# Performance work log

Hardware: AMD Instinct MI355X
Metric: run time of the kernel (lower is better)

Reference implementation:

```python
import jax, jax.numpy as jnp
import numpy as np

DIM = 1024
NUM_HEADS = 16
HEAD_DIM = DIM // NUM_HEADS
SCALE = HEAD_DIM ** -0.5


def setup_inputs() -> dict:
    key = jax.random.key(0)
    k1, k2, k3, k4 = jax.random.split(key, 4)
    x = jax.random.normal(k1, (4, 2048, DIM), dtype=jnp.float32)
    # torch nn.Linear(dim, 3*dim, bias=False): weight shape [3*dim, dim]
    w_qkv = jax.random.normal(k2, (3 * DIM, DIM), dtype=jnp.float32) * (DIM ** -0.5)
    # torch nn.Linear(dim, dim): weight [dim, dim], bias [dim]
    w_proj = jax.random.normal(k3, (DIM, DIM), dtype=jnp.float32) * (DIM ** -0.5)
    b_proj = jax.random.normal(k4, (DIM,), dtype=jnp.float32) * 0.01
    return {"x": x, "w_qkv": w_qkv, "w_proj": w_proj, "b_proj": b_proj}


def reference(x, w_qkv, w_proj, b_proj):
    B, N, C = x.shape
    # qkv: [B, N, 3*C] -> [3, B, H, N, Dh]
    qkv = (x @ w_qkv.T).reshape(B, N, 3, NUM_HEADS, HEAD_DIM)
    qkv = jnp.transpose(qkv, (2, 0, 3, 1, 4))
    q, k, v = qkv[0], qkv[1], qkv[2]
    # full score matrix, as in the original module
    attn = jnp.einsum("bhqd,bhkd->bhqk", q, k) * SCALE
    attn = jax.nn.softmax(attn, axis=-1)
    out = jnp.einsum("bhqk,bhkd->bhqd", attn, v)  # [B,H,N,Dh]
    out = jnp.transpose(out, (0, 2, 1, 3)).reshape(B, N, C)
    return out @ w_proj.T + b_proj
```

## Files before the change

kernel.cpp:

```cpp
#include <hip/hip_runtime.h>
#include <stdint.h>

#define DIM 1024
#define SEQ 2048
#define BATCH 4
#define ROWS (BATCH*SEQ)
#define QSCALE 0.1803368801111f

typedef __attribute__((ext_vector_type(8))) short bf16x8;
typedef __attribute__((ext_vector_type(4))) float f32x4;
typedef __attribute__((ext_vector_type(8))) _Float16 f16x8;
typedef __attribute__((ext_vector_type(2))) __fp16 fp16x2_raw;

#if __has_builtin(__builtin_amdgcn_exp2f)
#define EXP2F(x) __builtin_amdgcn_exp2f(x)
#else
#define EXP2F(x) __expf((x) * 0.69314718056f)
#endif

#define MFMA_BF16_K32(a,b,c) __builtin_amdgcn_mfma_f32_16x16x32_bf16(a,b,c,0,0,0)
#define MFMA_F16_K32(a,b,c)  __builtin_amdgcn_mfma_f32_16x16x32_f16(a,b,c,0,0,0)

__device__ __forceinline__ unsigned short f2bf(float f) {
  union { float f; unsigned int u; } v; v.f = f;
  unsigned int u = v.u;
  return (unsigned short)((u + 0x7FFFu + ((u >> 16) & 1u)) >> 16);
}

__device__ __forceinline__ unsigned short f2h(float f) {
  union { _Float16 h; unsigned short u; } v;
  v.h = (_Float16)f;
  return v.u;
}

__device__ __forceinline__ unsigned int pkrtz_bits(float lo, float hi) {
  union { fp16x2_raw h; unsigned int u; } v;
  v.h = __builtin_amdgcn_cvt_pkrtz(lo, hi);
  return v.u;
}

__device__ __forceinline__ void gload_lds16(const void* g, void* l) {
  __builtin_amdgcn_global_load_lds(
      (const __attribute__((address_space(1))) unsigned int*)g,
      (__attribute__((address_space(3))) unsigned int*)l,
      16, 0, 0);
}

__global__ void cast_all(const float* __restrict__ x,
                         const float* __restrict__ wq,
                         const float* __restrict__ wp,
                         unsigned short* __restrict__ xb,
                         unsigned short* __restrict__ wqb,
                         unsigned short* __restrict__ wpb) {
  const int i = (blockIdx.x * blockDim.x + threadIdx.x) * 4;
  const float* src;
  unsigned short* dst;
  int off;
  if (i < ROWS * DIM)                 { src = x;  dst = xb;  off = i; }
  else if (i < ROWS * DIM + 3 * DIM * DIM) { src = wq; dst = wqb; off = i - ROWS * DIM; }
  else                                { src = wp; dst = wpb; off = i - ROWS * DIM - 3 * DIM * DIM; }
  float4 f = *(const float4*)(src + off);
  ushort4 o;
  o.x = f2bf(f.x); o.y = f2bf(f.y); o.z = f2bf(f.z); o.w = f2bf(f.w);
  *(ushort4*)(dst + off) = o;
}

__global__ __launch_bounds__(256) void gemm_qkv(
    const unsigned short* __restrict__ A,
    const unsigned short* __restrict__ W,
    unsigned short* __restrict__ qb,
    unsigned short* __restrict__ kb,
    unsigned short* __restrict__ vtb) {
  const int K = DIM;
  __shared__ unsigned short Al[128 * 32];
  __shared__ unsigned short Wl[128 * 32];
  const int tid  = threadIdx.x;
  const int wave = tid >> 6, lane = tid & 63;
  const int quad = lane >> 4, l16 = lane & 15;
  const int m0 = blockIdx.y * 128, n0 = blockIdx.x * 128;
  const int wr = (wave >> 1) * 64, wc = (wave & 1) * 64;
  const int which = n0 >> 10;

  f32x4 acc[4][4];
#pragma unroll
  for (int i = 0; i < 4; i++)
#pragma unroll
    for (int j = 0; j < 4; j++) acc[i][j] = (f32x4)0.f;

  const int arow = wave * 16 + (lane >> 2);
  const int acol = (lane & 3) * 8;
  const unsigned short* Ag = A + (size_t)(m0 + arow) * K + acol;
  const unsigned short* Wg = W + (size_t)(n0 + arow) * K + acol;

  if (which < 2) {
    for (int kt = 0; kt < K; kt += 32) {
      __syncthreads();
#pragma unroll
      for (int i = 0; i < 2; i++) {
        gload_lds16((const void*)(Ag + (size_t)(i * 64) * K + kt), (void*)&Al[i * 2048 + wave * 512]);
        gload_lds16((const void*)(Wg + (size_t)(i * 64) * K + kt), (void*)&Wl[i * 2048 + wave * 512]);
      }
      __syncthreads();
      bf16x8 af[4], wf[4];
#pragma unroll
      for (int i = 0; i < 4; i++) {
        af[i] = *(const bf16x8*)&Al[(wr + i * 16 + l16) * 32 + quad * 8];
        wf[i] = *(const bf16x8*)&Wl[(wc + i * 16 + l16) * 32 + quad * 8];
      }
#pragma unroll
      for (int i = 0; i < 4; i++)
#pragma unroll
        for (int j = 0; j < 4; j++)
          acc[i][j] = __builtin_amdgcn_mfma_f32_16x16x32_bf16(wf[j], af[i], acc[i][j], 0, 0, 0);
    }
    const float sc = (which == 0) ? QSCALE : 1.f;
    unsigned short* base = (which == 0) ? qb : kb;
#pragma unroll
    for (int i = 0; i < 4; i++) {
      const int tok = m0 + wr + i * 16 + l16;
      const int b = tok >> 11, n = tok & 2047;
#pragma unroll
      for (int j = 0; j < 4; j++) {
        const int col0 = n0 + wc + j * 16 + quad * 4;
        const int h = (col0 >> 6) & 15, d = col0 & 63;
        ushort4 o4;
        o4.x = f2bf(acc[i][j][0] * sc); o4.y = f2bf(acc[i][j][1] * sc);
        o4.z = f2bf(acc[i][j][2] * sc); o4.w = f2bf(acc[i][j][3] * sc);
        *(ushort4*)&base[((size_t)(b * 16 + h) * SEQ + n) * 64 + d] = o4;
      }
    }
  } else {
    for (int kt = 0; kt < K; kt += 32) {
      __syncthreads();
#pragma unroll
      for (int i = 0; i < 2; i++) {
        gload_lds16((const void*)(Ag + (size_t)(i * 64) * K + kt), (void*)&Al[i * 2048 + wave * 512]);
        gload_lds16((const void*)(Wg + (size_t)(i * 64) * K + kt), (void*)&Wl[i * 2048 + wave * 512]);
      }
      __syncthreads();
      bf16x8 af[4], wf[4];
#pragma unroll
      for (int i = 0; i < 4; i++) {
        af[i] = *(const bf16x8*)&Al[(wr + i * 16 + l16) * 32 + quad * 8];
        wf[i] = *(const bf16x8*)&Wl[(wc + i * 16 + l16) * 32 + quad * 8];
      }
#pragma unroll
      for (int i = 0; i < 4; i++)
#pragma unroll
        for (int j = 0; j < 4; j++)
          acc[i][j] = __builtin_amdgcn_mfma_f32_16x16x32_bf16(af[i], wf[j], acc[i][j], 0, 0, 0);
    }
#pragma unroll
    for (int i = 0; i < 4; i++) {
      const int row = m0 + wr + i * 16 + quad * 4;
      const int b = row >> 11, n = row & 2047;
#pragma unroll
      for (int j = 0; j < 4; j++) {
        const int col = n0 + wc + j * 16 + l16;
        const int h = (col >> 6) & 15, d = col & 63;
        ushort4 o4;
        o4.x = f2h(acc[i][j][0]); o4.y = f2h(acc[i][j][1]);
        o4.z = f2h(acc[i][j][2]); o4.w = f2h(acc[i][j][3]);
        *(ushort4*)&vtb[((size_t)(b * 16 + h) * 64 + d) * SEQ + n] = o4;
      }
    }
  }
}

__global__ __launch_bounds__(256, 2) void attn_kernel(
    const unsigned short* __restrict__ qb,
    const unsigned short* __restrict__ kb,
    const unsigned short* __restrict__ vtb,
    unsigned short* __restrict__ out) {
  __shared__ unsigned short Kl[2][64 * 64];
  __shared__ unsigned short Vl[2][64 * 64];

  const int tid  = threadIdx.x;
  const int wave = tid >> 6, lane = tid & 63;
  const int quad = lane >> 4, l16 = lane & 15;
  const int bh    = blockIdx.x;
  const int qtile = blockIdx.y;
  const size_t qkbase = (size_t)bh * SEQ * 64;
  const int q0 = qtile * 256 + wave * 64;

  bf16x8 qf[4][2];
#pragma unroll
  for (int mi = 0; mi < 4; mi++)
#pragma unroll
    for (int kk = 0; kk < 2; kk++)
      qf[mi][kk] = *(const bf16x8*)&qb[qkbase + (size_t)(q0 + mi * 16 + l16) * 64 + kk * 32 + quad * 8];

  f32x4 o[4][4];
#pragma unroll
  for (int mi = 0; mi < 4; mi++)
#pragma unroll
    for (int nt = 0; nt < 4; nt++) o[mi][nt] = (f32x4)0.f;
  f32x4 lacc[4];
#pragma unroll
  for (int mi = 0; mi < 4; mi++) lacc[mi] = (f32x4)0.f;

  union { f16x8 v; unsigned int d[4]; } ones8;
#pragma unroll
  for (int j = 0; j < 4; j++) ones8.d[j] = 0x3C003C00u;

  const unsigned short* Kg = kb + qkbase;
  const unsigned short* Vg = vtb + (size_t)bh * 64 * SEQ;
  const int srow = tid >> 3;
  const int schk = tid & 7;
  const int swK = (srow & 3) | (((srow >> 3) & 1) << 2);
  const int swV = srow & 7;

  auto stage = [&](int kt, int buf) {
#pragma unroll
    for (int p = 0; p < 2; p++) {
      const int r = p * 32 + srow;
      gload_lds16((const void*)(Kg + (size_t)(kt + r) * 64 + (schk ^ swK) * 8),
                  (void*)&Kl[buf][p * 2048 + wave * 512]);
      gload_lds16((const void*)(Vg + (size_t)r * SEQ + kt + (schk ^ swV) * 8),
                  (void*)&Vl[buf][p * 2048 + wave * 512]);
    }
  };

  stage(0, 0);

  const int rbase = ((l16 >> 2) << 3) + (l16 & 3);
  const int sR = (l16 & 3) | (((l16 >> 2) & 1) << 2);

  int buf = 0;
  for (int kt = 0; kt < SEQ; kt += 64, buf ^= 1) {
    __syncthreads();
    if (kt + 64 < SEQ) stage(kt + 64, buf ^ 1);

#pragma unroll
    for (int kk = 0; kk < 2; kk++) {
      bf16x8 kf[2][2];
#pragma unroll
      for (int T = 0; T < 2; T++) {
        const int R = kk * 32 + rbase + 4 * T;
        kf[T][0] = *(const bf16x8*)&Kl[buf][R * 64 + ((quad ^ sR) << 3)];
        kf[T][1] = *(const bf16x8*)&Kl[buf][R * 64 + (((4 + quad) ^ sR) << 3)];
      }
      f16x8 vf[4];
#pragma unroll
      for (int nt = 0; nt < 4; nt++) {
        const int vr = nt * 16 + l16;
        vf[nt] = *(const f16x8*)&Vl[buf][vr * 64 + (((kk * 4 + quad) ^ (vr & 7)) << 3)];
      }
#pragma unroll
      for (int mi = 0; mi < 4; mi++) {
        f32x4 s0 = (f32x4)0.f, s1 = (f32x4)0.f;
        s0 = MFMA_BF16_K32(kf[0][0], qf[mi][0], s0);
        s0 = MFMA_BF16_K32(kf[0][1], qf[mi][1], s0);
        s1 = MFMA_BF16_K32(kf[1][0], qf[mi][0], s1);
        s1 = MFMA_BF16_K32(kf[1][1], qf[mi][1], s1);
        union { f16x8 v; unsigned int d[4]; } pu;
        pu.d[0] = pkrtz_bits(EXP2F(s0[0]), EXP2F(s0[1]));
        pu.d[1] = pkrtz_bits(EXP2F(s0[2]), EXP2F(s0[3]));
        pu.d[2] = pkrtz_bits(EXP2F(s1[0]), EXP2F(s1[1]));
        pu.d[3] = pkrtz_bits(EXP2F(s1[2]), EXP2F(s1[3]));
        lacc[mi] = MFMA_F16_K32(pu.v, ones8.v, lacc[mi]);
#pragma unroll
        for (int nt = 0; nt < 4; nt++)
          o[mi][nt] = MFMA_F16_K32(pu.v, vf[nt], o[mi][nt]);
      }
    }
  }

  const int h = bh & 15, b = bh >> 4;
#pragma unroll
  for (int mi = 0; mi < 4; mi++) {
    float inv[4];
#pragma unroll
    for (int r = 0; r < 4; r++) inv[r] = 1.f / lacc[mi][r];
#pragma unroll
    for (int nt = 0; nt < 4; nt++)
#pragma unroll
      for (int r = 0; r < 4; r++)
        out[((size_t)(b * SEQ + q0 + mi * 16 + quad * 4 + r)) * DIM + h * 64 + nt * 16 + l16] =
            f2bf(o[mi][nt][r] * inv[r]);
  }
}

__global__ __launch_bounds__(256) void gemm_proj(
    const unsigned short* __restrict__ A,
    const unsigned short* __restrict__ W,
    float* __restrict__ out,
    const float* __restrict__ bias) {
  const int N = DIM, K = DIM;
  __shared__ unsigned short Al[128 * 32];
  __shared__ unsigned short Wl[128 * 32];
  const int tid  = threadIdx.x;
  const int wave = tid >> 6, lane = tid & 63;
  const int quad = lane >> 4, l16 = lane & 15;
  const int m0 = blockIdx.y * 128, n0 = blockIdx.x * 128;
  const int wr = (wave >> 1) * 64, wc = (wave & 1) * 64;

  f32x4 acc[4][4];
#pragma unroll
  for (int i = 0; i < 4; i++)
#pragma unroll
    for (int j = 0; j < 4; j++) acc[i][j] = (f32x4)0.f;

  const int arow = wave * 16 + (lane >> 2);
  const int acol = (lane & 3) * 8;
  const unsigned short* Ag = A + (size_t)(m0 + arow) * K + acol;
  const unsigned short* Wg = W + (size_t)(n0 + arow) * K + acol;

  for (int kt = 0; kt < K; kt += 32) {
    __syncthreads();
#pragma unroll
    for (int i = 0; i < 2; i++) {
      gload_lds16((const void*)(Ag + (size_t)(i * 64) * K + kt), (void*)&Al[i * 2048 + wave * 512]);
      gload_lds16((const void*)(Wg + (size_t)(i * 64) * K + kt), (void*)&Wl[i * 2048 + wave * 512]);
    }
    __syncthreads();

    bf16x8 af[4], wf[4];
#pragma unroll
    for (int i = 0; i < 4; i++) {
      af[i] = *(const bf16x8*)&Al[(wr + i * 16 + l16) * 32 + quad * 8];
      wf[i] = *(const bf16x8*)&Wl[(wc + i * 16 + l16) * 32 + quad * 8];
    }
#pragma unroll
    for (int i = 0; i < 4; i++)
#pragma unroll
      for (int j = 0; j < 4; j++)
        acc[i][j] = __builtin_amdgcn_mfma_f32_16x16x32_bf16(af[i], wf[j], acc[i][j], 0, 0, 0);
  }

#pragma unroll
  for (int i = 0; i < 4; i++) {
    const int row = m0 + wr + i * 16 + quad * 4;
#pragma unroll
    for (int j = 0; j < 4; j++) {
      const int col = n0 + wc + j * 16 + l16;
      const float bv = bias[col];
#pragma unroll
      for (int r = 0; r < 4; r++)
        out[(size_t)(row + r) * N + col] = acc[i][j][r] + bv;
    }
  }
}

extern "C" void kernel_launch(void* const* d_in, const int* in_sizes, int n_in,
                              void* d_out, int out_size, void* d_ws, size_t ws_size,
                              hipStream_t stream) {
  const float* x      = (const float*)d_in[0];
  const float* w_qkv  = (const float*)d_in[1];
  const float* w_proj = (const float*)d_in[2];
  const float* b_proj = (const float*)d_in[3];
  float* outp = (float*)d_out;

  char* ws = (char*)d_ws;
  unsigned short* xb     = (unsigned short*)(ws);
  unsigned short* wqkvb  = (unsigned short*)(ws + (16u << 20));
  unsigned short* wprojb = (unsigned short*)(ws + (22u << 20));
  unsigned short* qb     = (unsigned short*)(ws + (24u << 20));
  unsigned short* kb     = (unsigned short*)(ws + (40u << 20));
  unsigned short* vtb    = (unsigned short*)(ws + (56u << 20));
  unsigned short* aout   = (unsigned short*)(ws + (72u << 20));

  const int total4 = (ROWS * DIM + 3 * DIM * DIM + DIM * DIM) / 4;
  cast_all<<<total4 / 256, 256, 0, stream>>>(x, w_qkv, w_proj, xb, wqkvb, wprojb);

  gemm_qkv<<<dim3(24, 64), 256, 0, stream>>>(xb, wqkvb, qb, kb, vtb);
  attn_kernel<<<dim3(64, 8), 256, 0, stream>>>(qb, kb, vtb, aout);
  gemm_proj<<<dim3(8, 64), 256, 0, stream>>>(aout, wprojb, outp, b_proj);
}
```

Measured before the change: 257.5 us.

## Rewrite QKV GEMM with 256x256 tiles, double-buffered LDS, swizzle and ping-pong

Replaces the 128x128 single-buffer QKV GEMM with a 512-thread kernel using 256x256 tiles, K-step 64, double-buffered XOR-swizzled LDS, interleaved staging of the next tiles between MFMA phases, s_setprio, and a grouped block-index remap. Q/K and V parts are split into two template launches so that the branch is resolved at compile time. This aims to raise MFMA utilisation and hide global load latency in the largest GEMM. In exchange it uses large LDS (128KB per block) and many accumulator registers, and it adds a second kernel launch.

```diff
diff --git a/kernel.cpp b/kernel.cpp
--- a/kernel.cpp
+++ b/kernel.cpp
@@ -65,102 +65,197 @@
   *(ushort4*)(dst + off) = o;
 }
 
-__global__ __launch_bounds__(256) void gemm_qkv(
+template<int SWAP>
+__device__ __forceinline__ f32x4 mm(bf16x8 a, bf16x8 b, f32x4 c) {
+  if constexpr (SWAP) return __builtin_amdgcn_mfma_f32_16x16x32_bf16(b, a, c, 0, 0, 0);
+  else                return __builtin_amdgcn_mfma_f32_16x16x32_bf16(a, b, c, 0, 0, 0);
+}
+
+template<int SWAP, int NTX>
+__global__ __launch_bounds__(512, 2) void gemm_qkv8(
     const unsigned short* __restrict__ A,
     const unsigned short* __restrict__ W,
     unsigned short* __restrict__ qb,
     unsigned short* __restrict__ kb,
     unsigned short* __restrict__ vtb) {
-  const int K = DIM;
-  __shared__ unsigned short Al[128 * 32];
-  __shared__ unsigned short Wl[128 * 32];
+  constexpr int K = DIM;
+  constexpr int NT = K / 64;
+  constexpr int N0B = SWAP ? 0 : 2048;
+  __shared__ unsigned short Al[2][256 * 64];
+  __shared__ unsigned short Bl[2][256 * 64];
+
   const int tid  = threadIdx.x;
   const int wave = tid >> 6, lane = tid & 63;
   const int quad = lane >> 4, l16 = lane & 15;
-  const int m0 = blockIdx.y * 128, n0 = blockIdx.x * 128;
-  const int wr = (wave >> 1) * 64, wc = (wave & 1) * 64;
-  const int which = n0 >> 10;
-
-  f32x4 acc[4][4];
-#pragma unroll
-  for (int i = 0; i < 4; i++)
-#pragma unroll
-    for (int j = 0; j < 4; j++) acc[i][j] = (f32x4)0.f;
-
-  const int arow = wave * 16 + (lane >> 2);
-  const int acol = (lane & 3) * 8;
-  const unsigned short* Ag = A + (size_t)(m0 + arow) * K + acol;
-  const unsigned short* Wg = W + (size_t)(n0 + arow) * K + acol;
-
-  if (which < 2) {
-    for (int kt = 0; kt < K; kt += 32) {
-      __syncthreads();
-#pragma unroll
-      for (int i = 0; i < 2; i++) {
-        gload_lds16((const void*)(Ag + (size_t)(i * 64) * K + kt), (void*)&Al[i * 2048 + wave * 512]);
-        gload_lds16((const void*)(Wg + (size_t)(i * 64) * K + kt), (void*)&Wl[i * 2048 + wave * 512]);
-      }
-      __syncthreads();
-      bf16x8 af[4], wf[4];
-#pragma unroll
-      for (int i = 0; i < 4; i++) {
-        af[i] = *(const bf16x8*)&Al[(wr + i * 16 + l16) * 32 + quad * 8];
-        wf[i] = *(const bf16x8*)&Wl[(wc + i * 16 + l16) * 32 + quad * 8];
-      }
-#pragma unroll
-      for (int i = 0; i < 4; i++)
-#pragma unroll
-        for (int j = 0; j < 4; j++)
-          acc[i][j] = __builtin_amdgcn_mfma_f32_16x16x32_bf16(wf[j], af[i], acc[i][j], 0, 0, 0);
-    }
-    const float sc = (which == 0) ? QSCALE : 1.f;
-    unsigned short* base = (which == 0) ? qb : kb;
-#pragma unroll
-    for (int i = 0; i < 4; i++) {
-      const int tok = m0 + wr + i * 16 + l16;
+  const int wm = wave >> 2, wn = wave & 3;
+
+  constexpr int nwg = NTX * 32;
+  int id = blockIdx.y * NTX + blockIdx.x;
+  id = (id & 7) * (nwg >> 3) + (id >> 3);
+  const int bx = id % NTX, by = id / NTX;
+  const int m0 = by * 256, n0 = N0B + bx * 256;
+
+  const int srow8 = lane >> 3;
+  const int schk  = (lane & 7) ^ srow8;
+  const unsigned short* Ast = A + (size_t)(m0 + wave * 8 + srow8) * K + (schk << 3);
+  const unsigned short* Bst = W + (size_t)(n0 + wave * 8 + srow8) * K + (schk << 3);
+
+  auto stg = [&](const unsigned short* g, int R0, int kt, unsigned short* l) {
+    gload_lds16((const void*)(g + (size_t)R0 * K + kt),
+                (void*)(l + (R0 + wave * 8) * 64));
+  };
+  auto ldf = [&](const unsigned short* base, int rb, int idx, int kk) -> bf16x8 {
+    const int r = rb + idx * 16 + l16;
+    return *(const bf16x8*)&base[r * 64 + (((kk * 4 + quad) ^ (l16 & 7)) << 3)];
+  };
+
+  f32x4 acc[8][4];
+#pragma unroll
+  for (int i = 0; i < 8; ++i)
+#pragma unroll
+    for (int j = 0; j < 4; ++j) acc[i][j] = (f32x4)0.f;
+
+  stg(Ast, 0, 0, Al[0]);  stg(Ast, 128, 0, Al[0]);
+  stg(Ast, 64, 0, Al[0]); stg(Ast, 192, 0, Al[0]);
+  stg(Bst, 0, 0, Bl[0]);  stg(Bst, 64, 0, Bl[0]);
+  stg(Bst, 128, 0, Bl[0]); stg(Bst, 192, 0, Bl[0]);
+  stg(Ast, 0, 64, Al[1]);  stg(Ast, 128, 64, Al[1]);
+  stg(Bst, 0, 64, Bl[1]);  stg(Bst, 64, 64, Bl[1]);
+  stg(Ast, 64, 64, Al[1]); stg(Ast, 192, 64, Al[1]);
+  asm volatile("s_waitcnt vmcnt(6)" ::: "memory");
+  __builtin_amdgcn_s_barrier();
+
+  bf16x8 af[4][2], bf[4][2];
+  int buf = 0;
+  for (int t = 0; t < NT; ++t, buf ^= 1) {
+    const unsigned short* Ac = Al[buf];
+    const unsigned short* Bc = Bl[buf];
+    unsigned short* Asg = Al[buf];
+    unsigned short* Bsg = Bl[buf];
+    const int kt2 = (t + 2) * 64;
+
+#pragma unroll
+    for (int mi = 0; mi < 4; ++mi) {
+      af[mi][0] = ldf(Ac, wm * 128, mi, 0);
+      af[mi][1] = ldf(Ac, wm * 128, mi, 1);
+    }
+#pragma unroll
+    for (int ni = 0; ni < 2; ++ni) {
+      bf[ni][0] = ldf(Bc, wn * 64, ni, 0);
+      bf[ni][1] = ldf(Bc, wn * 64, ni, 1);
+    }
+    if (t + 1 < NT) {
+      stg(Bst, 128, (t + 1) * 64, Bl[buf ^ 1]);
+      stg(Bst, 192, (t + 1) * 64, Bl[buf ^ 1]);
+    }
+    __builtin_amdgcn_s_barrier();
+    asm volatile("s_waitcnt lgkmcnt(0)" ::: "memory");
+    __builtin_amdgcn_s_setprio(1);
+#pragma unroll
+    for (int mi = 0; mi < 4; ++mi)
+#pragma unroll
+      for (int ni = 0; ni < 2; ++ni)
+#pragma unroll
+        for (int kk = 0; kk < 2; ++kk)
+          acc[mi][ni] = mm<SWAP>(af[mi][kk], bf[ni][kk], acc[mi][ni]);
+    __builtin_amdgcn_s_setprio(0);
+    __builtin_amdgcn_s_barrier();
+
+#pragma unroll
+    for (int ni = 2; ni < 4; ++ni) {
+      bf[ni][0] = ldf(Bc, wn * 64, ni, 0);
+      bf[ni][1] = ldf(Bc, wn * 64, ni, 1);
+    }
+    if (t + 2 < NT) {
+      stg(Ast, 0, kt2, Asg);
+      stg(Ast, 128, kt2, Asg);
+    }
+    __builtin_amdgcn_s_barrier();
+    asm volatile("s_waitcnt lgkmcnt(0)" ::: "memory");
+    __builtin_amdgcn_s_setprio(1);
+#pragma unroll
+    for (int mi = 0; mi < 4; ++mi)
+#pragma unroll
+      for (int ni = 2; ni < 4; ++ni)
+#pragma unroll
+        for (int kk = 0; kk < 2; ++kk)
+          acc[mi][ni] = mm<SWAP>(af[mi][kk], bf[ni][kk], acc[mi][ni]);
+    __builtin_amdgcn_s_setprio(0);
+    __builtin_amdgcn_s_barrier();
+
+#pragma unroll
+    for (int mi = 0; mi < 4; ++mi) {
+      af[mi][0] = ldf(Ac, wm * 128, mi + 4, 0);
+      af[mi][1] = ldf(Ac, wm * 128, mi + 4, 1);
+    }
+    if (t + 2 < NT) {
+      stg(Bst, 0, kt2, Bsg);
+      stg(Bst, 64, kt2, Bsg);
+    }
+    __builtin_amdgcn_s_barrier();
+    asm volatile("s_waitcnt lgkmcnt(0)" ::: "memory");
+    __builtin_amdgcn_s_setprio(1);
+#pragma unroll
+    for (int mi = 0; mi < 4; ++mi)
+#pragma unroll
+      for (int ni = 2; ni < 4; ++ni)
+#pragma unroll
+        for (int kk = 0; kk < 2; ++kk)
+          acc[mi + 4][ni] = mm<SWAP>(af[mi][kk], bf[ni][kk], acc[mi + 4][ni]);
+    __builtin_amdgcn_s_setprio(0);
+    __builtin_amdgcn_s_barrier();
+
+    if (t + 2 < NT) {
+      stg(Ast, 64, kt2, Asg);
+      stg(Ast, 192, kt2, Asg);
+      asm volatile("s_waitcnt vmcnt(6)" ::: "memory");
+    } else {
+      asm volatile("s_waitcnt vmcnt(0)" ::: "memory");
+    }
+    __builtin_amdgcn_s_barrier();
+    __builtin_amdgcn_s_setprio(1);
+#pragma unroll
+    for (int mi = 0; mi < 4; ++mi)
+#pragma unroll
+      for (int ni = 0; ni < 2; ++ni)
+#pragma unroll
+        for (int kk = 0; kk < 2; ++kk)
+          acc[mi + 4][ni] = mm<SWAP>(af[mi][kk], bf[ni][kk], acc[mi + 4][ni]);
+    __builtin_amdgcn_s_setprio(0);
+    __builtin_amdgcn_s_barrier();
+  }
+
+  if constexpr (SWAP) {
+    const float sc = (n0 < 1024) ? QSCALE : 1.f;
+    unsigned short* base = (n0 < 1024) ? qb : kb;
+#pragma unroll
+    for (int mi = 0; mi < 8; ++mi) {
+      const int tok = m0 + wm * 128 + mi * 16 + l16;
       const int b = tok >> 11, n = tok & 2047;
 #pragma unroll
-      for (int j = 0; j < 4; j++) {
-        const int col0 = n0 + wc + j * 16 + quad * 4;
-        const int h = (col0 >> 6) & 15, d = col0 & 63;
+      for (int ni = 0; ni < 4; ++ni) {
+        const int f0 = n0 + wn * 64 + ni * 16 + quad * 4;
+        const int h = (f0 >> 6) & 15, d = f0 & 63;
         ushort4 o4;
-        o4.x = f2bf(acc[i][j][0] * sc); o4.y = f2bf(acc[i][j][1] * sc);
-        o4.z = f2bf(acc[i][j][2] * sc); o4.w = f2bf(acc[i][j][3] * sc);
+        o4.x = f2bf(acc[mi][ni][0] * sc);
+        o4.y = f2bf(acc[mi][ni][1] * sc);
+        o4.z = f2bf(acc[mi][ni][2] * sc);
+        o4.w = f2bf(acc[mi][ni][3] * sc);
         *(ushort4*)&base[((size_t)(b * 16 + h) * SEQ + n) * 64 + d] = o4;
       }
     }
   } else {
-    for (int kt = 0; kt < K; kt += 32) {
-      __syncthreads();
-#pragma unroll
-      for (int i = 0; i < 2; i++) {
-        gload_lds16((const void*)(Ag + (size_t)(i * 64) * K + kt), (void*)&Al[i * 2048 + wave * 512]);
-        gload_lds16((const void*)(Wg + (size_t)(i * 64) * K + kt), (void*)&Wl[i * 2048 + wave * 512]);
-      }
-      __syncthreads();
-      bf16x8 af[4], wf[4];
-#pragma unroll
-      for (int i = 0; i < 4; i++) {
-        af[i] = *(const bf16x8*)&Al[(wr + i * 16 + l16) * 32 + quad * 8];
-        wf[i] = *(const bf16x8*)&Wl[(wc + i * 16 + l16) * 32 + quad * 8];
-      }
-#pragma unroll
-      for (int i = 0; i < 4; i++)
-#pragma unroll
-        for (int j = 0; j < 4; j++)
-          acc[i][j] = __builtin_amdgcn_mfma_f32_16x16x32_bf16(af[i], wf[j], acc[i][j], 0, 0, 0);
-    }
-#pragma unroll
-    for (int i = 0; i < 4; i++) {
-      const int row = m0 + wr + i * 16 + quad * 4;
+#pragma unroll
+    for (int mi = 0; mi < 8; ++mi) {
+      const int row = m0 + wm * 128 + mi * 16 + quad * 4;
       const int b = row >> 11, n = row & 2047;
 #pragma unroll
-      for (int j = 0; j < 4; j++) {
-        const int col = n0 + wc + j * 16 + l16;
+      for (int ni = 0; ni < 4; ++ni) {
+        const int col = n0 + wn * 64 + ni * 16 + l16;
         const int h = (col >> 6) & 15, d = col & 63;
         ushort4 o4;
-        o4.x = f2h(acc[i][j][0]); o4.y = f2h(acc[i][j][1]);
-        o4.z = f2h(acc[i][j][2]); o4.w = f2h(acc[i][j][3]);
+        o4.x = f2h(acc[mi][ni][0]); o4.y = f2h(acc[mi][ni][1]);
+        o4.z = f2h(acc[mi][ni][2]); o4.w = f2h(acc[mi][ni][3]);
         *(ushort4*)&vtb[((size_t)(b * 16 + h) * 64 + d) * SEQ + n] = o4;
       }
     }
@@ -363,7 +458,8 @@
   const int total4 = (ROWS * DIM + 3 * DIM * DIM + DIM * DIM) / 4;
   cast_all<<<total4 / 256, 256, 0, stream>>>(x, w_qkv, w_proj, xb, wqkvb, wprojb);
 
-  gemm_qkv<<<dim3(24, 64), 256, 0, stream>>>(xb, wqkvb, qb, kb, vtb);
+  gemm_qkv8<1, 8><<<dim3(8, 32), 512, 0, stream>>>(xb, wqkvb, qb, kb, vtb);
+  gemm_qkv8<0, 4><<<dim3(4, 32), 512, 0, stream>>>(xb, wqkvb, qb, kb, vtb);
   attn_kernel<<<dim3(64, 8), 256, 0, stream>>>(qb, kb, vtb, aout);
   gemm_proj<<<dim3(8, 64), 256, 0, stream>>>(aout, wprojb, outp, b_proj);
 }
```

Result: slower. 264.3 us (+2.6%).
